# Kernel optimization log

Measured on AMD Instinct MI355X. Metric: run time of the kernel, lower is better.

## Reference

```python
import jax, jax.numpy as jnp
import numpy as np

N_USERS = 100000
N_ITEMS = 200000
D = 64
N_LAYERS = 2
UI_EDGES = 3200000
SOC_EDGES = 1600000
EPS = 1e-5  # torch LayerNorm default


def setup_inputs() -> dict:
    key = jax.random.key(0)
    ks = jax.random.split(key, 10)
    user_emb = jax.random.normal(ks[0], (N_USERS, D), jnp.float32)
    item_emb = jax.random.normal(ks[1], (N_ITEMS, D), jnp.float32)
    ui_src = jax.random.randint(ks[2], (UI_EDGES,), 0, N_USERS, jnp.int32)
    ui_dst = jax.random.randint(ks[3], (UI_EDGES,), 0, N_ITEMS, jnp.int32)
    ui_val = jax.random.uniform(ks[4], (UI_EDGES,), jnp.float32)
    soc_src = jax.random.randint(ks[5], (SOC_EDGES,), 0, N_USERS, jnp.int32)
    soc_dst = jax.random.randint(ks[6], (SOC_EDGES,), 0, N_USERS, jnp.int32)
    soc_val = jax.random.uniform(ks[7], (SOC_EDGES,), jnp.float32)
    # learned params: shared ui_transform / social_transform Linear per layer, 2*n_layers LayerNorms
    W_ui = jax.random.normal(ks[8], (N_LAYERS, D, D), jnp.float32) / np.sqrt(D).astype(np.float32)
    b_ui = jnp.zeros((N_LAYERS, D), jnp.float32)
    W_soc = jax.random.normal(ks[9], (N_LAYERS, D, D), jnp.float32) / np.sqrt(D).astype(np.float32)
    b_soc = jnp.zeros((N_LAYERS, D), jnp.float32)
    ln_g = jnp.ones((2 * N_LAYERS, D), jnp.float32)
    ln_b = jnp.zeros((2 * N_LAYERS, D), jnp.float32)
    return dict(user_emb=user_emb, item_emb=item_emb, ui_src=ui_src, ui_dst=ui_dst,
                ui_val=ui_val, soc_src=soc_src, soc_dst=soc_dst, soc_val=soc_val,
                W_ui=W_ui, b_ui=b_ui, W_soc=W_soc, b_soc=b_soc, ln_g=ln_g, ln_b=ln_b)


def _layernorm(x, g, b):
    m = jnp.mean(x, axis=-1, keepdims=True)
    v = jnp.var(x, axis=-1, keepdims=True)  # biased, as torch LayerNorm
    return (x - m) * jax.lax.rsqrt(v + EPS) * g + b


def _spmm(src, dst, val, x, n_rows):
    # out[r] = sum_{e: src[e]==r} val[e] * x[dst[e]]  (COO SpMM)
    return jax.ops.segment_sum(val[:, None] * x[dst], src, num_segments=n_rows)


def reference(user_emb, item_emb, ui_src, ui_dst, ui_val, soc_src, soc_dst, soc_val,
              W_ui, b_ui, W_soc, b_soc, ln_g, ln_b):
    n_users = user_emb.shape[0]
    n_items = item_emb.shape[0]
    ui_list = [user_emb]
    soc_list = [user_emb]
    u, it, s = user_emb, item_emb, user_emb
    for i in range(N_LAYERS):
        # user-item bipartite propagation (item_user = transpose of user_item)
        agg_u = _spmm(ui_src, ui_dst, ui_val, it, n_users) @ W_ui[i] + b_ui[i]
        agg_i = _spmm(ui_dst, ui_src, ui_val, u, n_items) @ W_ui[i] + b_ui[i]
        u = _layernorm(u + agg_u, ln_g[2 * i], ln_b[2 * i])
        it = _layernorm(it + agg_i, ln_g[2 * i + 1], ln_b[2 * i + 1])
        ui_list.append(u)
        # social propagation (shares layer_norms[2i] params with user branch)
        agg_s = _spmm(soc_src, soc_dst, soc_val, s, n_users) @ W_soc[i] + b_soc[i]
        s = _layernorm(s + agg_s, ln_g[2 * i], ln_b[2 * i])
        soc_list.append(s)
    # dropout is identity in eval/reference mode
    return (jnp.stack(ui_list), jnp.stack(soc_list), it)
```

## Files before the change

kernel.cpp:

```cpp
#include <hip/hip_runtime.h>
#include <stdint.h>

static constexpr int NU    = 100000;
static constexpr int NI    = 200000;
static constexpr int D     = 64;
static constexpr int E_UI  = 3200000;
static constexpr int E_SOC = 1600000;
static constexpr int CH    = 8192;
static constexpr int BROWS = 512;
#define EPS_LN 1e-5f

typedef __attribute__((ext_vector_type(8))) short bf16x8;
typedef __attribute__((ext_vector_type(4))) float f32x4;

__device__ __forceinline__ unsigned short f2b(float f) {
    unsigned u = __float_as_uint(f);
    u = (u + 0x7FFFu + ((u >> 16) & 1u)) >> 16;
    return (unsigned short)u;
}
__device__ __forceinline__ float b2fs(unsigned short h) {
    return __uint_as_float((unsigned)h << 16);
}
__device__ __forceinline__ float b2f_lo(unsigned u) { return __uint_as_float(u << 16); }
__device__ __forceinline__ float b2f_hi(unsigned u) { return __uint_as_float(u & 0xFFFF0000u); }

__device__ __forceinline__ void fma8(float* a, float w, uint4 h) {
    a[0] += w * b2f_lo(h.x); a[1] += w * b2f_hi(h.x);
    a[2] += w * b2f_lo(h.y); a[3] += w * b2f_hi(h.y);
    a[4] += w * b2f_lo(h.z); a[5] += w * b2f_hi(h.z);
    a[6] += w * b2f_lo(h.w); a[7] += w * b2f_hi(h.w);
}

struct CntT { const int* rows; int E; int nblk; int nb; int* cnt; int blk0; };

__global__ void __launch_bounds__(256) bin_count3(CntT c0, CntT c1, CntT c2)
{
    __shared__ int hist[512];
    CntT c = (blockIdx.x >= (unsigned)c2.blk0) ? c2
           : (blockIdx.x >= (unsigned)c1.blk0) ? c1 : c0;
    int b = blockIdx.x - c.blk0, t = threadIdx.x;
    for (int i = t; i < c.nb; i += 256) hist[i] = 0;
    __syncthreads();
    int e0 = b * CH, e1 = min(c.E, e0 + CH);
    for (int e = e0 + t; e < e1; e += 256)
        atomicAdd(&hist[c.rows[e] >> 9], 1);
    __syncthreads();
    for (int i = t; i < c.nb; i += 256) c.cnt[i * c.nblk + b] = hist[i];
}

struct ScanT { const int* cnt; int n; int* bsum; int* ofs; int blk0; };

__global__ void scan_partial3(ScanT s0, ScanT s1, ScanT s2)
{
    __shared__ int lds[256];
    ScanT s = (blockIdx.x >= (unsigned)s2.blk0) ? s2
            : (blockIdx.x >= (unsigned)s1.blk0) ? s1 : s0;
    int bb = blockIdx.x - s.blk0;
    int i = bb * 256 + threadIdx.x;
    lds[threadIdx.x] = (i < s.n) ? s.cnt[i] : 0;
    __syncthreads();
    for (int off = 128; off > 0; off >>= 1) {
        if (threadIdx.x < off) lds[threadIdx.x] += lds[threadIdx.x + off];
        __syncthreads();
    }
    if (threadIdx.x == 0) s.bsum[bb] = lds[0];
}

__global__ void scan_bsums3(ScanT s0, ScanT s1, ScanT s2)
{
    __shared__ int lds[1024];
    ScanT s = (blockIdx.x == 2) ? s2 : (blockIdx.x == 1) ? s1 : s0;
    int nb = (s.n + 255) / 256;
    int t = threadIdx.x;
    int v = (t < nb) ? s.bsum[t] : 0;
    lds[t] = v;
    __syncthreads();
    for (int off = 1; off < 1024; off <<= 1) {
        int add = (t >= off) ? lds[t - off] : 0;
        __syncthreads();
        lds[t] += add;
        __syncthreads();
    }
    if (t < nb) s.bsum[t] = lds[t] - v;
}

__global__ void scan_out3(ScanT s0, ScanT s1, ScanT s2)
{
    __shared__ int lds[256];
    ScanT s = (blockIdx.x >= (unsigned)s2.blk0) ? s2
            : (blockIdx.x >= (unsigned)s1.blk0) ? s1 : s0;
    int bb = blockIdx.x - s.blk0;
    int i = bb * 256 + threadIdx.x;
    int v = (i < s.n) ? s.cnt[i] : 0;
    lds[threadIdx.x] = v;
    __syncthreads();
    for (int off = 1; off < 256; off <<= 1) {
        int add = (threadIdx.x >= off) ? lds[threadIdx.x - off] : 0;
        __syncthreads();
        lds[threadIdx.x] += add;
        __syncthreads();
    }
    if (i < s.n) s.ofs[i] = s.bsum[bb] + lds[threadIdx.x] - v;
}

struct ScatT { const int* rows; const int* idxs; const float* vals;
               int E; int nblk; const int* ofs; int nb; int2* binned; int blk0; };

__global__ void __launch_bounds__(256) bin_scatter3(ScatT c0, ScatT c1, ScatT c2)
{
    __shared__ int cur[512];
    ScatT c = (blockIdx.x >= (unsigned)c2.blk0) ? c2
            : (blockIdx.x >= (unsigned)c1.blk0) ? c1 : c0;
    int b = blockIdx.x - c.blk0, t = threadIdx.x;
    for (int i = t; i < c.nb; i += 256) cur[i] = c.ofs[i * c.nblk + b];
    __syncthreads();
    int e0 = b * CH, e1 = min(c.E, e0 + CH);
    for (int e = e0 + t; e < e1; e += 256) {
        int row = c.rows[e];
        int bucket = row >> 9;
        int slot = atomicAdd(&cur[bucket], 1);
        unsigned pack = ((unsigned)(row & 511) << 23) | (unsigned)c.idxs[e];
        c.binned[slot] = make_int2((int)pack, __float_as_int(c.vals[e]));
    }
}

struct FineT { const int2* binned; const int* ofs; int nblk; int nb;
               int E; int nrows; int* rowptr; int2* rec; int blk0; };

__global__ void __launch_bounds__(512) fine_scatter3(FineT c0, FineT c1, FineT c2)
{
    __shared__ int hist[512];
    __shared__ int cur[512];
    FineT c = (blockIdx.x >= (unsigned)c2.blk0) ? c2
            : (blockIdx.x >= (unsigned)c1.blk0) ? c1 : c0;
    int b = blockIdx.x - c.blk0, t = threadIdx.x;
    int beg = c.ofs[b * c.nblk];
    int end = (b + 1 < c.nb) ? c.ofs[(b + 1) * c.nblk] : c.E;

    hist[t] = 0;
    __syncthreads();
    for (int j = beg + t; j < end; j += 512)
        atomicAdd(&hist[((unsigned)c.binned[j].x) >> 23], 1);
    __syncthreads();
    int v = hist[t];
    for (int off = 1; off < 512; off <<= 1) {
        int add = (t >= off) ? hist[t - off] : 0;
        __syncthreads();
        hist[t] += add;
        __syncthreads();
    }
    int excl = hist[t] - v;
    cur[t] = excl;
    int grow = b * BROWS + t;
    if (grow <= c.nrows) c.rowptr[grow] = beg + excl;
    __syncthreads();
    for (int j = beg + t; j < end; j += 512) {
        int2 eb = c.binned[j];
        unsigned p = (unsigned)eb.x;
        int rl  = (int)(p >> 23);
        int idx = (int)(p & 0x7FFFFFu);
        int cc = atomicAdd(&cur[rl], 1);
        c.rec[beg + cc] = make_int2(idx, eb.y);
    }
}

__global__ void copy0_kernel(const float4* __restrict__ src, float4* __restrict__ a,
                             float4* __restrict__ b, int n4)
{
    int i = blockIdx.x * blockDim.x + threadIdx.x;
    if (i < n4) { float4 v = src[i]; a[i] = v; b[i] = v; }
}

struct TaskT {
    const float* x;
    unsigned short* tab;
    const float* W;
    int ntiles;
    int blk0;
    int nblk;
};

__device__ __forceinline__ void split_hi_lo(const f32x4 a, const f32x4 b,
                                            bf16x8& hi, bf16x8& lo)
{
    #pragma unroll
    for (int j = 0; j < 4; ++j) {
        unsigned short h = f2b(a[j]);
        hi[j] = (short)h;
        lo[j] = (short)f2b(a[j] - b2fs(h));
    }
    #pragma unroll
    for (int j = 0; j < 4; ++j) {
        unsigned short h = f2b(b[j]);
        hi[4 + j] = (short)h;
        lo[4 + j] = (short)f2b(b[j] - b2fs(h));
    }
}

__global__ void __launch_bounds__(256) btab3(TaskT t0, TaskT t1, TaskT t2)
{
    __shared__ float Wl[64 * 64];
    TaskT t = (blockIdx.x >= (unsigned)t2.blk0) ? t2
            : (blockIdx.x >= (unsigned)t1.blk0) ? t1 : t0;
    {
        const float4* W4 = (const float4*)t.W;
        float4* Wl4 = (float4*)Wl;
        for (int i = threadIdx.x; i < 1024; i += 256) Wl4[i] = W4[i];
    }
    __syncthreads();

    int wv   = threadIdx.x >> 6;
    int lane = threadIdx.x & 63;
    int g    = lane >> 4;
    int c    = lane & 15;

    bf16x8 Whi[2][4], Wlo[2][4];
    #pragma unroll
    for (int kt = 0; kt < 2; ++kt)
        #pragma unroll
        for (int nt = 0; nt < 4; ++nt)
            #pragma unroll
            for (int j = 0; j < 8; ++j) {
                float w = Wl[(kt * 32 + 8 * g + j) * 64 + nt * 16 + c];
                unsigned short h = f2b(w);
                Whi[kt][nt][j] = (short)h;
                Wlo[kt][nt][j] = (short)f2b(w - b2fs(h));
            }

    int stride = t.nblk * 4;
    for (int tile = (blockIdx.x - t.blk0) * 4 + wv; tile < t.ntiles; tile += stride) {
        int rowbase = tile * 16;
        const float* arow = t.x + (size_t)(rowbase + c) * 64 + 8 * g;
        f32x4 a00 = *(const f32x4*)(arow);
        f32x4 a01 = *(const f32x4*)(arow + 4);
        f32x4 a10 = *(const f32x4*)(arow + 32);
        f32x4 a11 = *(const f32x4*)(arow + 36);
        bf16x8 Ahi0, Alo0, Ahi1, Alo1;
        split_hi_lo(a00, a01, Ahi0, Alo0);
        split_hi_lo(a10, a11, Ahi1, Alo1);

        #pragma unroll
        for (int nt = 0; nt < 4; ++nt) {
            f32x4 z = {0.f, 0.f, 0.f, 0.f};
            z = __builtin_amdgcn_mfma_f32_16x16x32_bf16(Ahi0, Whi[0][nt], z, 0, 0, 0);
            z = __builtin_amdgcn_mfma_f32_16x16x32_bf16(Ahi1, Whi[1][nt], z, 0, 0, 0);
            z = __builtin_amdgcn_mfma_f32_16x16x32_bf16(Alo0, Whi[0][nt], z, 0, 0, 0);
            z = __builtin_amdgcn_mfma_f32_16x16x32_bf16(Alo1, Whi[1][nt], z, 0, 0, 0);
            z = __builtin_amdgcn_mfma_f32_16x16x32_bf16(Ahi0, Wlo[0][nt], z, 0, 0, 0);
            z = __builtin_amdgcn_mfma_f32_16x16x32_bf16(Ahi1, Wlo[1][nt], z, 0, 0, 0);
            #pragma unroll
            for (int reg = 0; reg < 4; ++reg)
                t.tab[(size_t)(rowbase + 4 * g + reg) * 64 + nt * 16 + c] = f2b(z[reg]);
        }
    }
}

struct TaskS {
    const unsigned short* gsrc;
    const float* xin;
    float* yout;
    const int* rowptr;
    const int2* recs;
    const float* bias;
    const float* gamma;
    const float* beta;
    int nrows;
    int blk0;
};

__global__ void __launch_bounds__(256) spmmln3(TaskS t0, TaskS t1, TaskS t2)
{
    TaskS t = (blockIdx.x >= (unsigned)t2.blk0) ? t2
            : (blockIdx.x >= (unsigned)t1.blk0) ? t1 : t0;
    int wid2 = (blockIdx.x - t.blk0) * 4 + (threadIdx.x >> 6);
    int lane = threadIdx.x & 63;
    int half = lane >> 5;
    int row  = wid2 * 2 + half;
    if (row >= t.nrows) return;

    int g4 = (lane >> 3) & 3;
    int l8 = lane & 7;

    float accA[8], accB[8];
    #pragma unroll
    for (int m = 0; m < 8; ++m) { accA[m] = 0.f; accB[m] = 0.f; }

    int beg = t.rowptr[row], end = t.rowptr[row + 1];
    int jb = beg;
    for (; jb + 16 <= end; jb += 16) {
        int2 r0 = t.recs[jb + g4];
        int2 r1 = t.recs[jb + 4 + g4];
        int2 r2 = t.recs[jb + 8 + g4];
        int2 r3 = t.recs[jb + 12 + g4];
        uint4 h0 = ((const uint4*)(t.gsrc + (size_t)r0.x * 64))[l8];
        uint4 h1 = ((const uint4*)(t.gsrc + (size_t)r1.x * 64))[l8];
        uint4 h2 = ((const uint4*)(t.gsrc + (size_t)r2.x * 64))[l8];
        uint4 h3 = ((const uint4*)(t.gsrc + (size_t)r3.x * 64))[l8];
        fma8(accA, __int_as_float(r0.y), h0);
        fma8(accB, __int_as_float(r1.y), h1);
        fma8(accA, __int_as_float(r2.y), h2);
        fma8(accB, __int_as_float(r3.y), h3);
    }
    if (jb < end) {
        int endm1 = end - 1;
        int e0 = jb + g4, e1 = jb + 4 + g4, e2 = jb + 8 + g4, e3 = jb + 12 + g4;
        int2 r0 = t.recs[min(e0, endm1)];
        int2 r1 = t.recs[min(e1, endm1)];
        int2 r2 = t.recs[min(e2, endm1)];
        int2 r3 = t.recs[min(e3, endm1)];
        if (e0 < end) { uint4 h = ((const uint4*)(t.gsrc + (size_t)r0.x * 64))[l8]; fma8(accA, __int_as_float(r0.y), h); }
        if (e1 < end) { uint4 h = ((const uint4*)(t.gsrc + (size_t)r1.x * 64))[l8]; fma8(accB, __int_as_float(r1.y), h); }
        if (e2 < end) { uint4 h = ((const uint4*)(t.gsrc + (size_t)r2.x * 64))[l8]; fma8(accA, __int_as_float(r2.y), h); }
        if (e3 < end) { uint4 h = ((const uint4*)(t.gsrc + (size_t)r3.x * 64))[l8]; fma8(accB, __int_as_float(r3.y), h); }
    }
    float acc[8];
    #pragma unroll
    for (int m = 0; m < 8; ++m) acc[m] = accA[m] + accB[m];
    #pragma unroll
    for (int off = 8; off <= 16; off <<= 1)
        #pragma unroll
        for (int m = 0; m < 8; ++m)
            acc[m] += __shfl_xor(acc[m], off);

    const float4* xi = (const float4*)(t.xin + (size_t)row * 64 + 8 * l8);
    const float4* bi = (const float4*)(t.bias + 8 * l8);
    float4 x0 = xi[0], x1 = xi[1];
    float4 bb0 = bi[0], bb1 = bi[1];
    float tv[8];
    tv[0] = x0.x + acc[0] + bb0.x; tv[1] = x0.y + acc[1] + bb0.y;
    tv[2] = x0.z + acc[2] + bb0.z; tv[3] = x0.w + acc[3] + bb0.w;
    tv[4] = x1.x + acc[4] + bb1.x; tv[5] = x1.y + acc[5] + bb1.y;
    tv[6] = x1.z + acc[6] + bb1.z; tv[7] = x1.w + acc[7] + bb1.w;

    float s = 0.f;
    #pragma unroll
    for (int m = 0; m < 8; ++m) s += tv[m];
    #pragma unroll
    for (int off = 1; off <= 4; off <<= 1) s += __shfl_xor(s, off);
    float mean = s * (1.0f / 64.0f);
    float q = 0.f;
    #pragma unroll
    for (int m = 0; m < 8; ++m) { float dv = tv[m] - mean; q += dv * dv; }
    #pragma unroll
    for (int off = 1; off <= 4; off <<= 1) q += __shfl_xor(q, off);
    float rs = rsqrtf(q * (1.0f / 64.0f) + EPS_LN);

    if (g4 == 0) {
        const float4* ga = (const float4*)(t.gamma + 8 * l8);
        const float4* be = (const float4*)(t.beta + 8 * l8);
        float4 g0 = ga[0], g1 = ga[1];
        float4 e0 = be[0], e1 = be[1];
        float4 y0, y1;
        y0.x = (tv[0] - mean) * rs * g0.x + e0.x;
        y0.y = (tv[1] - mean) * rs * g0.y + e0.y;
        y0.z = (tv[2] - mean) * rs * g0.z + e0.z;
        y0.w = (tv[3] - mean) * rs * g0.w + e0.w;
        y1.x = (tv[4] - mean) * rs * g1.x + e1.x;
        y1.y = (tv[5] - mean) * rs * g1.y + e1.y;
        y1.z = (tv[6] - mean) * rs * g1.z + e1.z;
        y1.w = (tv[7] - mean) * rs * g1.w + e1.w;
        float4* yo = (float4*)(t.yout + (size_t)row * 64 + 8 * l8);
        yo[0] = y0;
        yo[1] = y1;
    }
}

extern "C" void kernel_launch(void* const* d_in, const int* in_sizes, int n_in,
                              void* d_out, int out_size, void* d_ws, size_t ws_size,
                              hipStream_t stream)
{
    const float* user_emb = (const float*)d_in[0];
    const float* item_emb = (const float*)d_in[1];
    const int*   ui_src   = (const int*)d_in[2];
    const int*   ui_dst   = (const int*)d_in[3];
    const float* ui_val   = (const float*)d_in[4];
    const int*   soc_src  = (const int*)d_in[5];
    const int*   soc_dst  = (const int*)d_in[6];
    const float* soc_val  = (const float*)d_in[7];
    const float* W_ui     = (const float*)d_in[8];
    const float* b_ui     = (const float*)d_in[9];
    const float* W_soc    = (const float*)d_in[10];
    const float* b_soc    = (const float*)d_in[11];
    const float* ln_g     = (const float*)d_in[12];
    const float* ln_b     = (const float*)d_in[13];

    float* out     = (float*)d_out;
    float* out_ui  = out;
    float* out_soc = out + (size_t)3 * NU * D;
    float* out_it  = out + (size_t)6 * NU * D;

    const int NBU = (NU + BROWS - 1) / BROWS;
    const int NBI = (NI + BROWS - 1) / BROWS;
    const int BLK_UI  = (E_UI  + CH - 1) / CH;
    const int BLK_SOC = (E_SOC + CH - 1) / CH;

    const int N1 = NBU * BLK_UI;
    const int N2 = NBI * BLK_UI;
    const int N3 = NBU * BLK_SOC;
    const int SB1 = (N1 + 255) / 256, SB2 = (N2 + 255) / 256, SB3 = (N3 + 255) / 256;

    char* p = (char*)d_ws;
    auto take = [&](size_t bytes) { char* r = p; p += (bytes + 255) & ~(size_t)255; return r; };
    int2* rec_us = (int2*)take((size_t)E_UI * 8);
    int2* rec_ud = (int2*)take((size_t)E_UI * 8);
    int2* rec_ss = (int2*)take((size_t)E_SOC * 8);
    int2* bin1 = (int2*)take((size_t)E_UI * 8);
    int2* bin2 = (int2*)take((size_t)E_UI * 8);
    int2* bin3 = (int2*)take((size_t)E_SOC * 8);
    int*  rp_us  = (int*)take((size_t)(NU + 1) * 4);
    int*  rp_ud  = (int*)take((size_t)(NI + 1) * 4);
    int*  rp_ss  = (int*)take((size_t)(NU + 1) * 4);
    int*  cnt1 = (int*)take((size_t)N1 * 4);
    int*  cnt2 = (int*)take((size_t)N2 * 4);
    int*  cnt3 = (int*)take((size_t)N3 * 4);
    int*  ofs1 = (int*)take((size_t)N1 * 4);
    int*  ofs2 = (int*)take((size_t)N2 * 4);
    int*  ofs3 = (int*)take((size_t)N3 * 4);
    int*  bs1 = (int*)take(1024 * 4);
    int*  bs2 = (int*)take(1024 * 4);
    int*  bs3 = (int*)take(1024 * 4);
    unsigned short* twi = (unsigned short*)take((size_t)NU * D * 2);
    unsigned short* tws = (unsigned short*)take((size_t)NU * D * 2);
    unsigned short* twu = (unsigned short*)bin1;

    {
        CntT c1 { ui_src,  E_UI,  BLK_UI,  NBU, cnt1, 0 };
        CntT c2 { ui_dst,  E_UI,  BLK_UI,  NBI, cnt2, BLK_UI };
        CntT c3 { soc_src, E_SOC, BLK_SOC, NBU, cnt3, 2 * BLK_UI };
        bin_count3<<<2 * BLK_UI + BLK_SOC, 256, 0, stream>>>(c1, c2, c3);
    }
    {
        ScanT s1 { cnt1, N1, bs1, ofs1, 0 };
        ScanT s2 { cnt2, N2, bs2, ofs2, SB1 };
        ScanT s3 { cnt3, N3, bs3, ofs3, SB1 + SB2 };
        scan_partial3<<<SB1 + SB2 + SB3, 256, 0, stream>>>(s1, s2, s3);
        scan_bsums3<<<3, 1024, 0, stream>>>(s1, s2, s3);
        scan_out3<<<SB1 + SB2 + SB3, 256, 0, stream>>>(s1, s2, s3);
    }
    {
        ScatT c1 { ui_src,  ui_dst,  ui_val,  E_UI,  BLK_UI,  ofs1, NBU, bin1, 0 };
        ScatT c2 { ui_dst,  ui_src,  ui_val,  E_UI,  BLK_UI,  ofs2, NBI, bin2, BLK_UI };
        ScatT c3 { soc_src, soc_dst, soc_val, E_SOC, BLK_SOC, ofs3, NBU, bin3, 2 * BLK_UI };
        bin_scatter3<<<2 * BLK_UI + BLK_SOC, 256, 0, stream>>>(c1, c2, c3);
    }
    {
        FineT f1 { bin1, ofs1, BLK_UI,  NBU, E_UI,  NU, rp_us, rec_us, 0 };
        FineT f2 { bin2, ofs2, BLK_UI,  NBI, E_UI,  NI, rp_ud, rec_ud, NBU };
        FineT f3 { bin3, ofs3, BLK_SOC, NBU, E_SOC, NU, rp_ss, rec_ss, NBU + NBI };
        fine_scatter3<<<NBU + NBI + NBU, 512, 0, stream>>>(f1, f2, f3);
    }

    int n4 = NU * D / 4;
    copy0_kernel<<<(n4 + 255) / 256, 256, 0, stream>>>((const float4*)user_emb,
                                                       (float4*)out_ui, (float4*)out_soc, n4);

    const float* u0 = user_emb;
    float* u1 = out_ui + (size_t)NU * D;
    float* u2 = out_ui + (size_t)2 * NU * D;
    const float* s0 = user_emb;
    float* s1 = out_soc + (size_t)NU * D;
    float* s2 = out_soc + (size_t)2 * NU * D;

    int ublocks8 = (NU + 7) / 8;
    int iblocks8 = (NI + 7) / 8;
    int agrid    = iblocks8 + 2 * ublocks8;

    const int TB_I = 1040, TB_U = 520, TB_S = 520;
    int tgrid = TB_I + TB_U + TB_S;
    const int TIL_I = NI / 16, TIL_U = NU / 16;

    {
        TaskT ta { item_emb, twu, W_ui + 0 * 4096, TIL_I, 0, TB_I };
        TaskT tb { u0,       twi, W_ui + 0 * 4096, TIL_U, TB_I, TB_U };
        TaskT tc { u0,       tws, W_soc + 0 * 4096, TIL_U, TB_I + TB_U, TB_S };
        btab3<<<tgrid, 256, 0, stream>>>(ta, tb, tc);
    }
    {
        TaskS si { twi, item_emb, out_it, rp_ud, rec_ud, b_ui + 0 * 64,
                   ln_g + 1 * 64, ln_b + 1 * 64, NI, 0 };
        TaskS su { twu, u0, u1, rp_us, rec_us, b_ui + 0 * 64,
                   ln_g + 0 * 64, ln_b + 0 * 64, NU, iblocks8 };
        TaskS ss { tws, s0, s1, rp_ss, rec_ss, b_soc + 0 * 64,
                   ln_g + 0 * 64, ln_b + 0 * 64, NU, iblocks8 + ublocks8 };
        spmmln3<<<agrid, 256, 0, stream>>>(si, su, ss);
    }

    {
        TaskT ta { out_it, twu, W_ui + 1 * 4096, TIL_I, 0, TB_I };
        TaskT tb { u1,     twi, W_ui + 1 * 4096, TIL_U, TB_I, TB_U };
        TaskT tc { s1,     tws, W_soc + 1 * 4096, TIL_U, TB_I + TB_U, TB_S };
        btab3<<<tgrid, 256, 0, stream>>>(ta, tb, tc);
    }
    {
        TaskS si { twi, out_it, out_it, rp_ud, rec_ud, b_ui + 1 * 64,
                   ln_g + 3 * 64, ln_b + 3 * 64, NI, 0 };
        TaskS su { twu, u1, u2, rp_us, rec_us, b_ui + 1 * 64,
                   ln_g + 2 * 64, ln_b + 2 * 64, NU, iblocks8 };
        TaskS ss { tws, s1, s2, rp_ss, rec_ss, b_soc + 1 * 64,
                   ln_g + 2 * 64, ln_b + 2 * 64, NU, iblocks8 + ublocks8 };
        spmmln3<<<agrid, 256, 0, stream>>>(si, su, ss);
    }
}
```

Baseline: 680.7 us.

## Fuse edge counting with layer-0 transform and fold embedding copy into it

Merges the bin_count kernel with the first-layer dense-transform (btab) kernel into one launch, so histogram blocks and transform blocks run concurrently. The initial copy of user embeddings into the two output stacks is done inside the user transform tiles instead of a separate copy kernel. The item transform table now gets its own buffer rather than aliasing the binning scratch, since the transform now runs before binning finishes. This uses more workspace memory and gives the fused kernel more branching and register pressure.

```diff
diff --git a/kernel.cpp b/kernel.cpp
--- a/kernel.cpp
+++ b/kernel.cpp
@@ -32,144 +32,11 @@
 }
 
 struct CntT { const int* rows; int E; int nblk; int nb; int* cnt; int blk0; };
-
-__global__ void __launch_bounds__(256) bin_count3(CntT c0, CntT c1, CntT c2)
-{
-    __shared__ int hist[512];
-    CntT c = (blockIdx.x >= (unsigned)c2.blk0) ? c2
-           : (blockIdx.x >= (unsigned)c1.blk0) ? c1 : c0;
-    int b = blockIdx.x - c.blk0, t = threadIdx.x;
-    for (int i = t; i < c.nb; i += 256) hist[i] = 0;
-    __syncthreads();
-    int e0 = b * CH, e1 = min(c.E, e0 + CH);
-    for (int e = e0 + t; e < e1; e += 256)
-        atomicAdd(&hist[c.rows[e] >> 9], 1);
-    __syncthreads();
-    for (int i = t; i < c.nb; i += 256) c.cnt[i * c.nblk + b] = hist[i];
-}
-
 struct ScanT { const int* cnt; int n; int* bsum; int* ofs; int blk0; };
-
-__global__ void scan_partial3(ScanT s0, ScanT s1, ScanT s2)
-{
-    __shared__ int lds[256];
-    ScanT s = (blockIdx.x >= (unsigned)s2.blk0) ? s2
-            : (blockIdx.x >= (unsigned)s1.blk0) ? s1 : s0;
-    int bb = blockIdx.x - s.blk0;
-    int i = bb * 256 + threadIdx.x;
-    lds[threadIdx.x] = (i < s.n) ? s.cnt[i] : 0;
-    __syncthreads();
-    for (int off = 128; off > 0; off >>= 1) {
-        if (threadIdx.x < off) lds[threadIdx.x] += lds[threadIdx.x + off];
-        __syncthreads();
-    }
-    if (threadIdx.x == 0) s.bsum[bb] = lds[0];
-}
-
-__global__ void scan_bsums3(ScanT s0, ScanT s1, ScanT s2)
-{
-    __shared__ int lds[1024];
-    ScanT s = (blockIdx.x == 2) ? s2 : (blockIdx.x == 1) ? s1 : s0;
-    int nb = (s.n + 255) / 256;
-    int t = threadIdx.x;
-    int v = (t < nb) ? s.bsum[t] : 0;
-    lds[t] = v;
-    __syncthreads();
-    for (int off = 1; off < 1024; off <<= 1) {
-        int add = (t >= off) ? lds[t - off] : 0;
-        __syncthreads();
-        lds[t] += add;
-        __syncthreads();
-    }
-    if (t < nb) s.bsum[t] = lds[t] - v;
-}
-
-__global__ void scan_out3(ScanT s0, ScanT s1, ScanT s2)
-{
-    __shared__ int lds[256];
-    ScanT s = (blockIdx.x >= (unsigned)s2.blk0) ? s2
-            : (blockIdx.x >= (unsigned)s1.blk0) ? s1 : s0;
-    int bb = blockIdx.x - s.blk0;
-    int i = bb * 256 + threadIdx.x;
-    int v = (i < s.n) ? s.cnt[i] : 0;
-    lds[threadIdx.x] = v;
-    __syncthreads();
-    for (int off = 1; off < 256; off <<= 1) {
-        int add = (threadIdx.x >= off) ? lds[threadIdx.x - off] : 0;
-        __syncthreads();
-        lds[threadIdx.x] += add;
-        __syncthreads();
-    }
-    if (i < s.n) s.ofs[i] = s.bsum[bb] + lds[threadIdx.x] - v;
-}
-
 struct ScatT { const int* rows; const int* idxs; const float* vals;
                int E; int nblk; const int* ofs; int nb; int2* binned; int blk0; };
-
-__global__ void __launch_bounds__(256) bin_scatter3(ScatT c0, ScatT c1, ScatT c2)
-{
-    __shared__ int cur[512];
-    ScatT c = (blockIdx.x >= (unsigned)c2.blk0) ? c2
-            : (blockIdx.x >= (unsigned)c1.blk0) ? c1 : c0;
-    int b = blockIdx.x - c.blk0, t = threadIdx.x;
-    for (int i = t; i < c.nb; i += 256) cur[i] = c.ofs[i * c.nblk + b];
-    __syncthreads();
-    int e0 = b * CH, e1 = min(c.E, e0 + CH);
-    for (int e = e0 + t; e < e1; e += 256) {
-        int row = c.rows[e];
-        int bucket = row >> 9;
-        int slot = atomicAdd(&cur[bucket], 1);
-        unsigned pack = ((unsigned)(row & 511) << 23) | (unsigned)c.idxs[e];
-        c.binned[slot] = make_int2((int)pack, __float_as_int(c.vals[e]));
-    }
-}
-
 struct FineT { const int2* binned; const int* ofs; int nblk; int nb;
                int E; int nrows; int* rowptr; int2* rec; int blk0; };
-
-__global__ void __launch_bounds__(512) fine_scatter3(FineT c0, FineT c1, FineT c2)
-{
-    __shared__ int hist[512];
-    __shared__ int cur[512];
-    FineT c = (blockIdx.x >= (unsigned)c2.blk0) ? c2
-            : (blockIdx.x >= (unsigned)c1.blk0) ? c1 : c0;
-    int b = blockIdx.x - c.blk0, t = threadIdx.x;
-    int beg = c.ofs[b * c.nblk];
-    int end = (b + 1 < c.nb) ? c.ofs[(b + 1) * c.nblk] : c.E;
-
-    hist[t] = 0;
-    __syncthreads();
-    for (int j = beg + t; j < end; j += 512)
-        atomicAdd(&hist[((unsigned)c.binned[j].x) >> 23], 1);
-    __syncthreads();
-    int v = hist[t];
-    for (int off = 1; off < 512; off <<= 1) {
-        int add = (t >= off) ? hist[t - off] : 0;
-        __syncthreads();
-        hist[t] += add;
-        __syncthreads();
-    }
-    int excl = hist[t] - v;
-    cur[t] = excl;
-    int grow = b * BROWS + t;
-    if (grow <= c.nrows) c.rowptr[grow] = beg + excl;
-    __syncthreads();
-    for (int j = beg + t; j < end; j += 512) {
-        int2 eb = c.binned[j];
-        unsigned p = (unsigned)eb.x;
-        int rl  = (int)(p >> 23);
-        int idx = (int)(p & 0x7FFFFFu);
-        int cc = atomicAdd(&cur[rl], 1);
-        c.rec[beg + cc] = make_int2(idx, eb.y);
-    }
-}
-
-__global__ void copy0_kernel(const float4* __restrict__ src, float4* __restrict__ a,
-                             float4* __restrict__ b, int n4)
-{
-    int i = blockIdx.x * blockDim.x + threadIdx.x;
-    if (i < n4) { float4 v = src[i]; a[i] = v; b[i] = v; }
-}
 
 struct TaskT {
     const float* x;
@@ -178,6 +45,8 @@
     int ntiles;
     int blk0;
     int nblk;
+    float* cpyA;
+    float* cpyB;
 };
 
 __device__ __forceinline__ void split_hi_lo(const f32x4 a, const f32x4 b,
@@ -197,11 +66,8 @@
     }
 }
 
-__global__ void __launch_bounds__(256) btab3(TaskT t0, TaskT t1, TaskT t2)
-{
-    __shared__ float Wl[64 * 64];
-    TaskT t = (blockIdx.x >= (unsigned)t2.blk0) ? t2
-            : (blockIdx.x >= (unsigned)t1.blk0) ? t1 : t0;
+__device__ __forceinline__ void btab_device(const TaskT& t, float* Wl, int bidx)
+{
     {
         const float4* W4 = (const float4*)t.W;
         float4* Wl4 = (float4*)Wl;
@@ -228,13 +94,21 @@
             }
 
     int stride = t.nblk * 4;
-    for (int tile = (blockIdx.x - t.blk0) * 4 + wv; tile < t.ntiles; tile += stride) {
+    for (int tile = (bidx - t.blk0) * 4 + wv; tile < t.ntiles; tile += stride) {
         int rowbase = tile * 16;
         const float* arow = t.x + (size_t)(rowbase + c) * 64 + 8 * g;
         f32x4 a00 = *(const f32x4*)(arow);
         f32x4 a01 = *(const f32x4*)(arow + 4);
         f32x4 a10 = *(const f32x4*)(arow + 32);
         f32x4 a11 = *(const f32x4*)(arow + 36);
+        if (t.cpyA) {
+            float* dA = t.cpyA + (size_t)(rowbase + c) * 64 + 8 * g;
+            *(f32x4*)(dA)      = a00; *(f32x4*)(dA + 4)  = a01;
+            *(f32x4*)(dA + 32) = a10; *(f32x4*)(dA + 36) = a11;
+            float* dB = t.cpyB + (size_t)(rowbase + c) * 64 + 8 * g;
+            *(f32x4*)(dB)      = a00; *(f32x4*)(dB + 4)  = a01;
+            *(f32x4*)(dB + 32) = a10; *(f32x4*)(dB + 36) = a11;
+        }
         bf16x8 Ahi0, Alo0, Ahi1, Alo1;
         split_hi_lo(a00, a01, Ahi0, Alo0);
         split_hi_lo(a10, a11, Ahi1, Alo1);
@@ -252,6 +126,145 @@
             for (int reg = 0; reg < 4; ++reg)
                 t.tab[(size_t)(rowbase + 4 * g + reg) * 64 + nt * 16 + c] = f2b(z[reg]);
         }
+    }
+}
+
+__global__ void __launch_bounds__(256) front_l0(CntT c1, CntT c2, CntT c3, int nCnt,
+                                                TaskT ta, TaskT tb, TaskT tc)
+{
+    __shared__ float Wl[64 * 64];
+    if ((int)blockIdx.x < nCnt) {
+        int* hist = (int*)Wl;
+        CntT c = ((int)blockIdx.x >= c3.blk0) ? c3
+               : ((int)blockIdx.x >= c2.blk0) ? c2 : c1;
+        int b = blockIdx.x - c.blk0, t = threadIdx.x;
+        for (int i = t; i < c.nb; i += 256) hist[i] = 0;
+        __syncthreads();
+        int e0 = b * CH, e1 = min(c.E, e0 + CH);
+        for (int e = e0 + t; e < e1; e += 256)
+            atomicAdd(&hist[c.rows[e] >> 9], 1);
+        __syncthreads();
+        for (int i = t; i < c.nb; i += 256) c.cnt[i * c.nblk + b] = hist[i];
+    } else {
+        int bidx = blockIdx.x - nCnt;
+        const TaskT& t = (bidx >= tc.blk0) ? tc : (bidx >= tb.blk0) ? tb : ta;
+        btab_device(t, Wl, bidx);
+    }
+}
+
+__global__ void __launch_bounds__(256) btab3(TaskT t0, TaskT t1, TaskT t2)
+{
+    __shared__ float Wl[64 * 64];
+    const TaskT& t = ((int)blockIdx.x >= t2.blk0) ? t2
+                   : ((int)blockIdx.x >= t1.blk0) ? t1 : t0;
+    btab_device(t, Wl, blockIdx.x);
+}
+
+__global__ void scan_partial3(ScanT s0, ScanT s1, ScanT s2)
+{
+    __shared__ int lds[256];
+    ScanT s = (blockIdx.x >= (unsigned)s2.blk0) ? s2
+            : (blockIdx.x >= (unsigned)s1.blk0) ? s1 : s0;
+    int bb = blockIdx.x - s.blk0;
+    int i = bb * 256 + threadIdx.x;
+    lds[threadIdx.x] = (i < s.n) ? s.cnt[i] : 0;
+    __syncthreads();
+    for (int off = 128; off > 0; off >>= 1) {
+        if (threadIdx.x < off) lds[threadIdx.x] += lds[threadIdx.x + off];
+        __syncthreads();
+    }
+    if (threadIdx.x == 0) s.bsum[bb] = lds[0];
+}
+
+__global__ void scan_bsums3(ScanT s0, ScanT s1, ScanT s2)
+{
+    __shared__ int lds[1024];
+    ScanT s = (blockIdx.x == 2) ? s2 : (blockIdx.x == 1) ? s1 : s0;
+    int nb = (s.n + 255) / 256;
+    int t = threadIdx.x;
+    int v = (t < nb) ? s.bsum[t] : 0;
+    lds[t] = v;
+    __syncthreads();
+    for (int off = 1; off < 1024; off <<= 1) {
+        int add = (t >= off) ? lds[t - off] : 0;
+        __syncthreads();
+        lds[t] += add;
+        __syncthreads();
+    }
+    if (t < nb) s.bsum[t] = lds[t] - v;
+}
+
+__global__ void scan_out3(ScanT s0, ScanT s1, ScanT s2)
+{
+    __shared__ int lds[256];
+    ScanT s = (blockIdx.x >= (unsigned)s2.blk0) ? s2
+            : (blockIdx.x >= (unsigned)s1.blk0) ? s1 : s0;
+    int bb = blockIdx.x - s.blk0;
+    int i = bb * 256 + threadIdx.x;
+    int v = (i < s.n) ? s.cnt[i] : 0;
+    lds[threadIdx.x] = v;
+    __syncthreads();
+    for (int off = 1; off < 256; off <<= 1) {
+        int add = (threadIdx.x >= off) ? lds[threadIdx.x - off] : 0;
+        __syncthreads();
+        lds[threadIdx.x] += add;
+        __syncthreads();
+    }
+    if (i < s.n) s.ofs[i] = s.bsum[bb] + lds[threadIdx.x] - v;
+}
+
+__global__ void __launch_bounds__(256) bin_scatter3(ScatT c0, ScatT c1, ScatT c2)
+{
+    __shared__ int cur[512];
+    ScatT c = (blockIdx.x >= (unsigned)c2.blk0) ? c2
+            : (blockIdx.x >= (unsigned)c1.blk0) ? c1 : c0;
+    int b = blockIdx.x - c.blk0, t = threadIdx.x;
+    for (int i = t; i < c.nb; i += 256) cur[i] = c.ofs[i * c.nblk + b];
+    __syncthreads();
+    int e0 = b * CH, e1 = min(c.E, e0 + CH);
+    for (int e = e0 + t; e < e1; e += 256) {
+        int row = c.rows[e];
+        int bucket = row >> 9;
+        int slot = atomicAdd(&cur[bucket], 1);
+        unsigned pack = ((unsigned)(row & 511) << 23) | (unsigned)c.idxs[e];
+        c.binned[slot] = make_int2((int)pack, __float_as_int(c.vals[e]));
+    }
+}
+
+__global__ void __launch_bounds__(512) fine_scatter3(FineT c0, FineT c1, FineT c2)
+{
+    __shared__ int hist[512];
+    __shared__ int cur[512];
+    FineT c = (blockIdx.x >= (unsigned)c2.blk0) ? c2
+            : (blockIdx.x >= (unsigned)c1.blk0) ? c1 : c0;
+    int b = blockIdx.x - c.blk0, t = threadIdx.x;
+    int beg = c.ofs[b * c.nblk];
+    int end = (b + 1 < c.nb) ? c.ofs[(b + 1) * c.nblk] : c.E;
+
+    hist[t] = 0;
+    __syncthreads();
+    for (int j = beg + t; j < end; j += 512)
+        atomicAdd(&hist[((unsigned)c.binned[j].x) >> 23], 1);
+    __syncthreads();
+    int v = hist[t];
+    for (int off = 1; off < 512; off <<= 1) {
+        int add = (t >= off) ? hist[t - off] : 0;
+        __syncthreads();
+        hist[t] += add;
+        __syncthreads();
+    }
+    int excl = hist[t] - v;
+    cur[t] = excl;
+    int grow = b * BROWS + t;
+    if (grow <= c.nrows) c.rowptr[grow] = beg + excl;
+    __syncthreads();
+    for (int j = beg + t; j < end; j += 512) {
+        int2 eb = c.binned[j];
+        unsigned p = (unsigned)eb.x;
+        int rl  = (int)(p >> 23);
+        int idx = (int)(p & 0x7FFFFFu);
+        int cc = atomicAdd(&cur[rl], 1);
+        c.rec[beg + cc] = make_int2(idx, eb.y);
     }
 }
 
@@ -421,38 +434,11 @@
     int*  bs3 = (int*)take(1024 * 4);
     unsigned short* twi = (unsigned short*)take((size_t)NU * D * 2);
     unsigned short* tws = (unsigned short*)take((size_t)NU * D * 2);
-    unsigned short* twu = (unsigned short*)bin1;
-
-    {
-        CntT c1 { ui_src,  E_UI,  BLK_UI,  NBU, cnt1, 0 };
-        CntT c2 { ui_dst,  E_UI,  BLK_UI,  NBI, cnt2, BLK_UI };
-        CntT c3 { soc_src, E_SOC, BLK_SOC, NBU, cnt3, 2 * BLK_UI };
-        bin_count3<<<2 * BLK_UI + BLK_SOC, 256, 0, stream>>>(c1, c2, c3);
-    }
-    {
-        ScanT s1 { cnt1, N1, bs1, ofs1, 0 };
-        ScanT s2 { cnt2, N2, bs2, ofs2, SB1 };
-        ScanT s3 { cnt3, N3, bs3, ofs3, SB1 + SB2 };
-        scan_partial3<<<SB1 + SB2 + SB3, 256, 0, stream>>>(s1, s2, s3);
-        scan_bsums3<<<3, 1024, 0, stream>>>(s1, s2, s3);
-        scan_out3<<<SB1 + SB2 + SB3, 256, 0, stream>>>(s1, s2, s3);
-    }
-    {
-        ScatT c1 { ui_src,  ui_dst,  ui_val,  E_UI,  BLK_UI,  ofs1, NBU, bin1, 0 };
-        ScatT c2 { ui_dst,  ui_src,  ui_val,  E_UI,  BLK_UI,  ofs2, NBI, bin2, BLK_UI };
-        ScatT c3 { soc_src, soc_dst, soc_val, E_SOC, BLK_SOC, ofs3, NBU, bin3, 2 * BLK_UI };
-        bin_scatter3<<<2 * BLK_UI + BLK_SOC, 256, 0, stream>>>(c1, c2, c3);
-    }
-    {
-        FineT f1 { bin1, ofs1, BLK_UI,  NBU, E_UI,  NU, rp_us, rec_us, 0 };
-        FineT f2 { bin2, ofs2, BLK_UI,  NBI, E_UI,  NI, rp_ud, rec_ud, NBU };
-        FineT f3 { bin3, ofs3, BLK_SOC, NBU, E_SOC, NU, rp_ss, rec_ss, NBU + NBI };
-        fine_scatter3<<<NBU + NBI + NBU, 512, 0, stream>>>(f1, f2, f3);
-    }
-
-    int n4 = NU * D / 4;
-    copy0_kernel<<<(n4 + 255) / 256, 256, 0, stream>>>((const float4*)user_emb,
-                                                       (float4*)out_ui, (float4*)out_soc, n4);
+    unsigned short* twu = (unsigned short*)take((size_t)NI * D * 2);
+
+    const int TB_I = 1040, TB_U = 520, TB_S = 520;
+    int tgrid = TB_I + TB_U + TB_S;
+    const int TIL_I = NI / 16, TIL_U = NU / 16;
 
     const float* u0 = user_emb;
     float* u1 = out_ui + (size_t)NU * D;
@@ -461,20 +447,41 @@
     float* s1 = out_soc + (size_t)NU * D;
     float* s2 = out_soc + (size_t)2 * NU * D;
 
+    int nCnt = 2 * BLK_UI + BLK_SOC;
+    {
+        CntT c1 { ui_src,  E_UI,  BLK_UI,  NBU, cnt1, 0 };
+        CntT c2 { ui_dst,  E_UI,  BLK_UI,  NBI, cnt2, BLK_UI };
+        CntT c3 { soc_src, E_SOC, BLK_SOC, NBU, cnt3, 2 * BLK_UI };
+        TaskT ta { item_emb, twu, W_ui + 0 * 4096, TIL_I, 0, TB_I, nullptr, nullptr };
+        TaskT tb { u0,       twi, W_ui + 0 * 4096, TIL_U, TB_I, TB_U, out_ui, out_soc };
+        TaskT tc { u0,       tws, W_soc + 0 * 4096, TIL_U, TB_I + TB_U, TB_S, nullptr, nullptr };
+        front_l0<<<nCnt + tgrid, 256, 0, stream>>>(c1, c2, c3, nCnt, ta, tb, tc);
+    }
+    {
+        ScanT s1s { cnt1, N1, bs1, ofs1, 0 };
+        ScanT s2s { cnt2, N2, bs2, ofs2, SB1 };
+        ScanT s3s { cnt3, N3, bs3, ofs3, SB1 + SB2 };
+        scan_partial3<<<SB1 + SB2 + SB3, 256, 0, stream>>>(s1s, s2s, s3s);
+        scan_bsums3<<<3, 1024, 0, stream>>>(s1s, s2s, s3s);
+        scan_out3<<<SB1 + SB2 + SB3, 256, 0, stream>>>(s1s, s2s, s3s);
+    }
+    {
+        ScatT c1 { ui_src,  ui_dst,  ui_val,  E_UI,  BLK_UI,  ofs1, NBU, bin1, 0 };
+        ScatT c2 { ui_dst,  ui_src,  ui_val,  E_UI,  BLK_UI,  ofs2, NBI, bin2, BLK_UI };
+        ScatT c3 { soc_src, soc_dst, soc_val, E_SOC, BLK_SOC, ofs3, NBU, bin3, 2 * BLK_UI };
+        bin_scatter3<<<2 * BLK_UI + BLK_SOC, 256, 0, stream>>>(c1, c2, c3);
+    }
+    {
+        FineT f1 { bin1, ofs1, BLK_UI,  NBU, E_UI,  NU, rp_us, rec_us, 0 };
+        FineT f2 { bin2, ofs2, BLK_UI,  NBI, E_UI,  NI, rp_ud, rec_ud, NBU };
+        FineT f3 { bin3, ofs3, BLK_SOC, NBU, E_SOC, NU, rp_ss, rec_ss, NBU + NBI };
+        fine_scatter3<<<NBU + NBI + NBU, 512, 0, stream>>>(f1, f2, f3);
+    }
+
     int ublocks8 = (NU + 7) / 8;
     int iblocks8 = (NI + 7) / 8;
     int agrid    = iblocks8 + 2 * ublocks8;
 
-    const int TB_I = 1040, TB_U = 520, TB_S = 520;
-    int tgrid = TB_I + TB_U + TB_S;
-    const int TIL_I = NI / 16, TIL_U = NU / 16;
-
-    {
-        TaskT ta { item_emb, twu, W_ui + 0 * 4096, TIL_I, 0, TB_I };
-        TaskT tb { u0,       twi, W_ui + 0 * 4096, TIL_U, TB_I, TB_U };
-        TaskT tc { u0,       tws, W_soc + 0 * 4096, TIL_U, TB_I + TB_U, TB_S };
-        btab3<<<tgrid, 256, 0, stream>>>(ta, tb, tc);
-    }
     {
         TaskS si { twi, item_emb, out_it, rp_ud, rec_ud, b_ui + 0 * 64,
                    ln_g + 1 * 64, ln_b + 1 * 64, NI, 0 };
@@ -486,9 +493,9 @@
     }
 
     {
-        TaskT ta { out_it, twu, W_ui + 1 * 4096, TIL_I, 0, TB_I };
-        TaskT tb { u1,     twi, W_ui + 1 * 4096, TIL_U, TB_I, TB_U };
-        TaskT tc { s1,     tws, W_soc + 1 * 4096, TIL_U, TB_I + TB_U, TB_S };
+        TaskT ta { out_it, twu, W_ui + 1 * 4096, TIL_I, 0, TB_I, nullptr, nullptr };
+        TaskT tb { u1,     twi, W_ui + 1 * 4096, TIL_U, TB_I, TB_U, nullptr, nullptr };
+        TaskT tc { s1,     tws, W_soc + 1 * 4096, TIL_U, TB_I + TB_U, TB_S, nullptr, nullptr };
         btab3<<<tgrid, 256, 0, stream>>>(ta, tb, tc);
     }
     {
```

Measured after the change: 695.8 us. +2.2%, slower.
